# Kernel optimization log

Measured on AMD Instinct MI355X. Metric: run time of the kernel, lower is better.

The kernel has to match this reference:

```python
import jax, jax.numpy as jnp
import numpy as np
from jax import lax

B, L, CIN, COUT, K, H, W = 16, 4, 256, 256, 3, 32, 32
STRIDE, PAD, DIL = 1, 1, 1


def setup_inputs() -> dict:
    key = jax.random.key(0)
    ks = jax.random.split(key, 7)
    x = jax.random.normal(ks[0], (B, L, CIN, H, W), dtype=jnp.float32)
    # base conv weight, stored squeezed from torch shape (1,1,COUT,CIN,K,K)
    weight = jax.random.normal(ks[1], (COUT, CIN, K, K), dtype=jnp.float32) * 0.02
    bias = jax.random.normal(ks[2], (COUT,), dtype=jnp.float32) * 0.02
    # temporalconv: Conv3d(CIN, CIN, (3,1,1)) -> 1D conv over temporal axis
    tconv_w = jax.random.normal(ks[3], (CIN, CIN, 3), dtype=jnp.float32) * 0.02
    tconv_b = jax.random.normal(ks[4], (CIN,), dtype=jnp.float32) * 0.02
    # fc: Conv3d(CIN, 1, (3,1,1))
    fc_w = jax.random.normal(ks[5], (1, CIN, 3), dtype=jnp.float32) * 0.02
    fc_b = jax.random.normal(ks[6], (1,), dtype=jnp.float32) * 0.02
    return {"x": x, "weight": weight, "bias": bias, "tconv_w": tconv_w,
            "tconv_b": tconv_b, "fc_w": fc_w, "fc_b": fc_b}


def _conv1d(inp, w):
    # inp: (b, c_in, t), w: (c_out, c_in, 3), VALID padding -> (b, c_out, t-2)
    return lax.conv_general_dilated(inp, w, window_strides=(1,), padding='VALID',
                                    dimension_numbers=('NCH', 'OIH', 'NCH'))


def reference(x, weight, bias, tconv_w, tconv_b, fc_w, fc_b):
    b, l, c, h, w = x.shape
    # AdaptiveAvgPool3d((None,1,1)) after permute -> spatial global mean: (b, c, l)
    pooled = x.mean(axis=(3, 4)).transpose(0, 2, 1)
    # duplicate first frame twice along temporal axis: (b, c, l+2)
    allxet = jnp.concatenate([pooled[:, :, :1], pooled[:, :, :1], pooled], axis=2)
    calib = _conv1d(allxet, tconv_w) + tconv_b[None, :, None]      # (b, c, l)
    gate = _conv1d(allxet, fc_w) + fc_b[None, :, None]             # (b, 1, l)
    # per-(sample,frame) channel scale on input channels of base weight
    scale = (calib + 1.0).transpose(0, 2, 1)                       # (b, l, c)
    fw = weight[None, None] * scale[:, :, None, :, None, None]     # (b, l, COUT, CIN, K, K)
    fb = bias[None, None, :] * (gate[:, 0, :] + 1.0)[:, :, None]   # (b, l, COUT)
    n = b * l
    xN = x.reshape(n, c, h, w)
    fwN = fw.reshape(n, COUT, c, K, K)
    pad2 = [(PAD, PAD), (PAD, PAD)]

    def conv_one(xi, wi):  # per-sample conv: groups=b*l trick -> vmapped conv
        return lax.conv_general_dilated(xi[None], wi, (STRIDE, STRIDE), pad2,
                                        rhs_dilation=(DIL, DIL),
                                        dimension_numbers=('NCHW', 'OIHW', 'NCHW'))[0]

    out = jax.vmap(conv_one)(xN, fwN)                              # (n, COUT, H', W')
    out = out + fb.reshape(n, COUT)[:, :, None, None]
    return out
```

## Files before the change

### kernel.cpp

```cpp
#include <hip/hip_runtime.h>
#include <hip/hip_bf16.h>

#define CIN 256
#define COUT 256
#define HH 32
#define WW 32
#define LL 4
#define NN 64

typedef unsigned short u16;
typedef __attribute__((ext_vector_type(8))) short short8;
typedef __attribute__((ext_vector_type(4))) float f32x4;

typedef const __attribute__((address_space(1))) void gvoid_t;
typedef __attribute__((address_space(3))) void svoid_t;

static __device__ __forceinline__ u16 f2bf(float f) {
    __hip_bfloat16 h = __float2bfloat16(f);
    return *reinterpret_cast<u16*>(&h);
}
static __device__ __forceinline__ float bf2f(u16 b) {
    unsigned int u = ((unsigned int)b) << 16;
    return __uint_as_float(u);
}

__global__ __launch_bounds__(256) void prep_kernel(const float* __restrict__ x,
                                                   const float* __restrict__ weight,
                                                   const float* __restrict__ tconv_w,
                                                   float* __restrict__ pooled,
                                                   u16* __restrict__ xb,
                                                   u16* __restrict__ wb,
                                                   float* __restrict__ twt) {
    int bx = blockIdx.x;
    int tid = threadIdx.x;
    __shared__ float red[4][8];

    if (bx < 2048) {
        int n = bx >> 5, ko = bx & 31;
        int lane = tid & 63, wave = tid >> 6;
        const float* xn = x + ((size_t)n * CIN + ko * 8) * (HH * WW);

        float psum[8];
        #pragma unroll
        for (int ci = 0; ci < 8; ci++) psum[ci] = 0.f;

        size_t base = ((size_t)n * 32 + ko) * (34 * 34);
        #pragma unroll
        for (int k = 0; k < 4; k++) {
            int pos = k * 256 + tid;
            int h = pos >> 5, w = pos & 31;
            short8 u;
            #pragma unroll
            for (int ci = 0; ci < 8; ci++) {
                float f = xn[ci * (HH * WW) + pos];
                psum[ci] += f;
                u[ci] = (short)f2bf(f);
            }
            *(short8*)(xb + (base + (size_t)(h + 1) * 34 + (w + 1)) * 8) = u;
        }
        if (tid < 132) {
            int cell = tid;
            int hp, wp;
            if (cell < 34)       { hp = 0;              wp = cell; }
            else if (cell < 68)  { hp = 33;             wp = cell - 34; }
            else if (cell < 100) { hp = cell - 68 + 1;  wp = 0; }
            else                 { hp = cell - 100 + 1; wp = 33; }
            short8 z = (short8){0, 0, 0, 0, 0, 0, 0, 0};
            *(short8*)(xb + (base + (size_t)hp * 34 + wp) * 8) = z;
        }
        #pragma unroll
        for (int ci = 0; ci < 8; ci++) {
            float s = psum[ci];
            #pragma unroll
            for (int off = 32; off > 0; off >>= 1) s += __shfl_down(s, off, 64);
            if (lane == 0) red[wave][ci] = s;
        }
        __syncthreads();
        if (tid < 8) {
            pooled[n * CIN + ko * 8 + tid] =
                (red[0][tid] + red[1][tid] + red[2][tid] + red[3][tid]) * (1.0f / (HH * WW));
        }
    } else if (bx < 2304) {
        int co = bx - 2048;
        int ci = tid;
        #pragma unroll
        for (int k = 0; k < 9; k++) {
            u16 v = f2bf(weight[((size_t)co * CIN + ci) * 9 + k]);
            size_t unit = ((size_t)k * 32 + (ci >> 3)) * COUT + co;
            wb[unit * 8 + (ci & 7)] = v;
        }
    } else {
        int co = bx - 2304;
        #pragma unroll
        for (int r = 0; r < 3; r++) {
            int idx = r * 256 + tid;
            int ci = idx / 3, k = idx - ci * 3;
            twt[((size_t)k * 256 + ci) * 256 + co] = tconv_w[(size_t)co * 768 + idx];
        }
    }
}

__global__ __launch_bounds__(256) void calib2_kernel(const float* __restrict__ pooled,
                                                     const float* __restrict__ twt,
                                                     const float* __restrict__ tconv_b,
                                                     const float* __restrict__ fc_w,
                                                     const float* __restrict__ fc_b,
                                                     float* __restrict__ scale,
                                                     float* __restrict__ gmul) {
    int n = blockIdx.x >> 2, coq = blockIdx.x & 3;
    int b = n / LL, t = n % LL;
    int i0 = max(t - 2, 0), i1 = max(t - 1, 0), i2 = t;
    __shared__ float p[3][CIN];
    __shared__ float red[4][64];
    int tid = threadIdx.x;
    p[0][tid] = pooled[(b * LL + i0) * CIN + tid];
    p[1][tid] = pooled[(b * LL + i1) * CIN + tid];
    p[2][tid] = pooled[(b * LL + i2) * CIN + tid];
    __syncthreads();
    int co = coq * 64 + (tid & 63);
    int c0 = (tid >> 6) * 64;
    float acc = 0.f;
    #pragma unroll 4
    for (int i = 0; i < 64; i++) {
        int ci = c0 + i;
        acc += p[0][ci] * twt[(size_t)(0 * 256 + ci) * 256 + co]
             + p[1][ci] * twt[(size_t)(1 * 256 + ci) * 256 + co]
             + p[2][ci] * twt[(size_t)(2 * 256 + ci) * 256 + co];
    }
    red[tid >> 6][tid & 63] = acc;
    __syncthreads();
    if (tid < 64) {
        float a = red[0][tid] + red[1][tid] + red[2][tid] + red[3][tid];
        scale[n * CIN + coq * 64 + tid] = a + tconv_b[coq * 64 + tid] + 1.0f;
    }
    if (coq == 0) {
        const float* fw = fc_w + tid * 3;
        float g = p[0][tid] * fw[0] + p[1][tid] * fw[1] + p[2][tid] * fw[2];
        #pragma unroll
        for (int off = 32; off > 0; off >>= 1) g += __shfl_down(g, off, 64);
        __shared__ float gw[4];
        if ((tid & 63) == 0) gw[tid >> 6] = g;
        __syncthreads();
        if (tid == 0) gmul[n] = gw[0] + gw[1] + gw[2] + gw[3] + fc_b[0] + 1.0f;
    }
}

#define AUNITS 2376
#define BUNITS 2560

__global__ __launch_bounds__(256, 2) void conv_mfma_kernel(
    const u16* __restrict__ xb, const u16* __restrict__ wb,
    const float* __restrict__ scale,
    const float* __restrict__ bias, const float* __restrict__ gmul,
    float* __restrict__ out) {
    int blk = (blockIdx.x & 7) * 64 + (blockIdx.x >> 3);
    int n = blk >> 3, cog = (blk >> 1) & 3, pg = blk & 1;
    int r0 = pg * 16;
    int tid = threadIdx.x;
    int lane = tid & 63, wave = tid >> 6;
    int l15 = lane & 15, l4 = lane >> 4;
    int w4 = wave * 4;

    __shared__ short8 Alds[AUNITS];
    __shared__ short8 Blds[BUNITS];
    __shared__ float scale_lds[CIN];

    scale_lds[tid] = scale[n * CIN + tid];

    f32x4 acc[4][4][2];
    #pragma unroll
    for (int m = 0; m < 4; m++)
        #pragma unroll
        for (int r = 0; r < 4; r++)
            #pragma unroll
            for (int ch = 0; ch < 2; ch++) acc[m][r][ch] = (f32x4){0.f, 0.f, 0.f, 0.f};

    int a_src = wave * 256 + cog * 64 + lane;
    int b_off[10];
    #pragma unroll
    for (int r = 0; r < 10; r++) {
        int u = r * 256 + tid;
        int ue = u < 2455 ? u : 2455;
        int k8 = ue / 614;
        int rem = ue - k8 * 614;
        if (rem > 611) rem = 611;
        b_off[r] = k8 * 1156 + rem;
    }
    int b_base0 = n * 36992 + r0 * 34;

    for (int kc = 0; kc < 8; kc++) {
        __syncthreads();
        #pragma unroll
        for (int r = 0; r < 10; r++) {
            size_t gu = (size_t)(b_base0 + kc * 4624 + b_off[r]);
            __builtin_amdgcn_global_load_lds((gvoid_t*)(xb + gu * 8),
                (svoid_t*)&Blds[r * 256 + wave * 64], 16, 0, 0);
        }
        f32x4 s_lo = *(const f32x4*)&scale_lds[kc * 32 + wave * 8];
        f32x4 s_hi = *(const f32x4*)&scale_lds[kc * 32 + wave * 8 + 4];
        short8 wv[9];
        #pragma unroll
        for (int r = 0; r < 9; r++) {
            size_t gu = (size_t)(r * 8192 + kc * 1024 + a_src);
            wv[r] = *(const short8*)(wb + gu * 8);
        }
        #pragma unroll
        for (int r = 0; r < 9; r++) {
            short8 o;
            #pragma unroll
            for (int e = 0; e < 8; e++) {
                float s = (e < 4) ? s_lo[e] : s_hi[e - 4];
                o[e] = (short)f2bf(bf2f((u16)wv[r][e]) * s);
            }
            Alds[(r * 4 + wave) * 66 + lane] = o;
        }
        __syncthreads();

        #pragma unroll
        for (int dw = 0; dw < 3; dw++) {
            short8 bfr[6][2];
            #pragma unroll
            for (int j = 0; j < 6; j++)
                #pragma unroll
                for (int ch = 0; ch < 2; ch++) {
                    int u = l4 * 614 + (w4 + j) * 34 + ch * 16 + l15 + dw;
                    bfr[j][ch] = Blds[u];
                }
            #pragma unroll
            for (int dh = 0; dh < 3; dh++) {
                int tap = dh * 3 + dw;
                #pragma unroll
                for (int m = 0; m < 4; m++) {
                    int ua = (tap * 4 + l4) * 66 + m * 16 + l15;
                    short8 af = Alds[ua];
                    #pragma unroll
                    for (int r = 0; r < 4; r++)
                        #pragma unroll
                        for (int ch = 0; ch < 2; ch++)
                            acc[m][r][ch] = __builtin_amdgcn_mfma_f32_16x16x32_bf16(
                                af, bfr[r + dh][ch], acc[m][r][ch], 0, 0, 0);
                }
            }
        }
    }

    float gm = gmul[n];
    #pragma unroll
    for (int m = 0; m < 4; m++) {
        #pragma unroll
        for (int r = 0; r < 4; r++) {
            int orow = r0 + w4 + r;
            #pragma unroll
            for (int ch = 0; ch < 2; ch++) {
                #pragma unroll
                for (int j = 0; j < 4; j++) {
                    int co = cog * 64 + m * 16 + l4 * 4 + j;
                    out[(((size_t)n * COUT + co) * HH + orow) * WW + ch * 16 + l15] =
                        acc[m][r][ch][j] + bias[co] * gm;
                }
            }
        }
    }
}

__global__ __launch_bounds__(256) void pool_kernel(const float* __restrict__ x,
                                                   float* __restrict__ pooled) {
    int blk = blockIdx.x;
    const float* src = x + (size_t)blk * (HH * WW);
    int tid = threadIdx.x;
    float4 v = ((const float4*)src)[tid];
    float s = v.x + v.y + v.z + v.w;
    #pragma unroll
    for (int off = 32; off > 0; off >>= 1) s += __shfl_down(s, off, 64);
    __shared__ float ws[4];
    if ((tid & 63) == 0) ws[tid >> 6] = s;
    __syncthreads();
    if (tid == 0) pooled[blk] = (ws[0] + ws[1] + ws[2] + ws[3]) * (1.0f / (HH * WW));
}

__global__ __launch_bounds__(256) void calib_kernel(const float* __restrict__ pooled,
                                                    const float* __restrict__ tconv_w,
                                                    const float* __restrict__ tconv_b,
                                                    const float* __restrict__ fc_w,
                                                    const float* __restrict__ fc_b,
                                                    float* __restrict__ scale,
                                                    float* __restrict__ gmul) {
    int n = blockIdx.x;
    int b = n / LL, t = n % LL;
    int i0 = max(t - 2, 0), i1 = max(t - 1, 0), i2 = t;
    __shared__ float p[3][CIN];
    int tid = threadIdx.x;
    p[0][tid] = pooled[(b * LL + i0) * CIN + tid];
    p[1][tid] = pooled[(b * LL + i1) * CIN + tid];
    p[2][tid] = pooled[(b * LL + i2) * CIN + tid];
    __syncthreads();
    float acc = 0.f;
    for (int ci = 0; ci < CIN; ci++) {
        const float* w = tconv_w + ((size_t)tid * CIN + ci) * 3;
        acc += p[0][ci] * w[0] + p[1][ci] * w[1] + p[2][ci] * w[2];
    }
    scale[n * CIN + tid] = acc + tconv_b[tid] + 1.0f;
    const float* fw = fc_w + tid * 3;
    float g = p[0][tid] * fw[0] + p[1][tid] * fw[1] + p[2][tid] * fw[2];
    #pragma unroll
    for (int off = 32; off > 0; off >>= 1) g += __shfl_down(g, off, 64);
    __shared__ float gw[4];
    if ((tid & 63) == 0) gw[tid >> 6] = g;
    __syncthreads();
    if (tid == 0) gmul[n] = gw[0] + gw[1] + gw[2] + gw[3] + fc_b[0] + 1.0f;
}

__global__ __launch_bounds__(256) void conv_kernel(const float* __restrict__ x,
                                                   const float* __restrict__ weight,
                                                   const float* __restrict__ bias,
                                                   const float* __restrict__ scale,
                                                   const float* __restrict__ gmul,
                                                   float* __restrict__ out) {
    int blk = blockIdx.x;
    int n   = blk >> 5;
    int cog = (blk >> 3) & 3;
    int rg  = blk & 7;
    int co_base  = cog * 64;
    int row_base = rg * 4;
    int tid = threadIdx.x;
    int c   = tid & 31;
    int sub = tid >> 5;

    __shared__ float xin[6][34];
    __shared__ float wsh[9][65];

    float acc[8][4];
    #pragma unroll
    for (int j = 0; j < 8; j++)
        #pragma unroll
        for (int g = 0; g < 4; g++) acc[j][g] = 0.f;

    const float* xn = x + (size_t)n * CIN * HH * WW;

    for (int ci = 0; ci < CIN; ci++) {
        if (tid < 204) {
            float s = scale[n * CIN + ci];
            int lr = tid / 34, lc = tid % 34;
            int gr = row_base - 1 + lr, gc = lc - 1;
            float v = 0.f;
            if (gr >= 0 && gr < HH && gc >= 0 && gc < WW)
                v = xn[(size_t)ci * (HH * WW) + gr * WW + gc] * s;
            xin[lr][lc] = v;
        }
        for (int idx = tid; idx < 576; idx += 256) {
            int co = idx / 9, k = idx % 9;
            wsh[k][co] = weight[(size_t)(co_base + co) * (CIN * 9) + ci * 9 + k];
        }
        __syncthreads();
        float xr[6][3];
        #pragma unroll
        for (int r = 0; r < 6; r++)
            #pragma unroll
            for (int kw = 0; kw < 3; kw++) xr[r][kw] = xin[r][c + kw];
        #pragma unroll
        for (int j = 0; j < 8; j++) {
            float wv[9];
            #pragma unroll
            for (int k = 0; k < 9; k++) wv[k] = wsh[k][sub * 8 + j];
            #pragma unroll
            for (int g = 0; g < 4; g++)
                #pragma unroll
                for (int kh = 0; kh < 3; kh++)
                    #pragma unroll
                    for (int kw = 0; kw < 3; kw++)
                        acc[j][g] += xr[g + kh][kw] * wv[kh * 3 + kw];
        }
        __syncthreads();
    }
    float gm = gmul[n];
    #pragma unroll
    for (int j = 0; j < 8; j++) {
        int co = co_base + sub * 8 + j;
        float fb = bias[co] * gm;
        #pragma unroll
        for (int g = 0; g < 4; g++)
            out[(((size_t)n * COUT + co) * HH + (row_base + g)) * WW + c] = acc[j][g] + fb;
    }
}

extern "C" void kernel_launch(void* const* d_in, const int* in_sizes, int n_in,
                              void* d_out, int out_size, void* d_ws, size_t ws_size,
                              hipStream_t stream) {
    const float* x       = (const float*)d_in[0];
    const float* weight  = (const float*)d_in[1];
    const float* bias    = (const float*)d_in[2];
    const float* tconv_w = (const float*)d_in[3];
    const float* tconv_b = (const float*)d_in[4];
    const float* fc_w    = (const float*)d_in[5];
    const float* fc_b    = (const float*)d_in[6];
    float* out = (float*)d_out;

    char* wsb = (char*)d_ws;
    float* pooled = (float*)wsb;
    float* scale  = pooled + NN * CIN;
    float* gmul   = scale + NN * CIN;
    const size_t XB_OFF = 131328;
    const size_t XB_BYTES = (size_t)NN * 32 * 34 * 34 * 8 * 2;
    const size_t WB_OFF = XB_OFF + XB_BYTES;
    const size_t WB_BYTES = (size_t)9 * 32 * COUT * 8 * 2;
    const size_t TWT_OFF = WB_OFF + WB_BYTES;
    const size_t TWT_BYTES = (size_t)3 * 256 * 256 * 4;
    u16* xb = (u16*)(wsb + XB_OFF);
    u16* wb = (u16*)(wsb + WB_OFF);
    float* twt = (float*)(wsb + TWT_OFF);

    if (ws_size >= TWT_OFF + TWT_BYTES) {
        prep_kernel<<<2560, 256, 0, stream>>>(x, weight, tconv_w, pooled, xb, wb, twt);
        calib2_kernel<<<NN * 4, 256, 0, stream>>>(pooled, twt, tconv_b, fc_w, fc_b, scale, gmul);
        conv_mfma_kernel<<<NN * 4 * 2, 256, 0, stream>>>(xb, wb, scale, bias, gmul, out);
    } else {
        pool_kernel<<<NN * CIN, 256, 0, stream>>>(x, pooled);
        calib_kernel<<<NN, 256, 0, stream>>>(pooled, tconv_w, tconv_b, fc_w, fc_b, scale, gmul);
        conv_kernel<<<NN * 32, 256, 0, stream>>>(x, weight, bias, scale, gmul, out);
    }
}
```

Baseline: 93.07 us.

## Fold channel scale into input activations instead of per-sample weights

The per-(sample,frame) input-channel scale is now applied to the activations while they are converted to padded bf16, in a new kernel that runs after the calibration kernel. The first prep kernel only pools. The conv kernel no longer rescales weights into LDS each K-chunk and reads the shared bf16 weights straight from global memory into MFMA operands. This removes per-block weight scaling and the A tile in LDS, which frees LDS and conversion ALU work. The cost is a second full read of x in an extra launch, and A fragments now come from global or L2 memory inside the MFMA loop.

```diff
diff --git a/kernel.cpp b/kernel.cpp
--- a/kernel.cpp
+++ b/kernel.cpp
@@ -19,18 +19,13 @@
     __hip_bfloat16 h = __float2bfloat16(f);
     return *reinterpret_cast<u16*>(&h);
 }
-static __device__ __forceinline__ float bf2f(u16 b) {
-    unsigned int u = ((unsigned int)b) << 16;
-    return __uint_as_float(u);
-}
-
-__global__ __launch_bounds__(256) void prep_kernel(const float* __restrict__ x,
-                                                   const float* __restrict__ weight,
-                                                   const float* __restrict__ tconv_w,
-                                                   float* __restrict__ pooled,
-                                                   u16* __restrict__ xb,
-                                                   u16* __restrict__ wb,
-                                                   float* __restrict__ twt) {
+
+__global__ __launch_bounds__(256) void pool_prep_kernel(const float* __restrict__ x,
+                                                        const float* __restrict__ weight,
+                                                        const float* __restrict__ tconv_w,
+                                                        float* __restrict__ pooled,
+                                                        u16* __restrict__ wb,
+                                                        float* __restrict__ twt) {
     int bx = blockIdx.x;
     int tid = threadIdx.x;
     __shared__ float red[4][8];
@@ -39,34 +34,11 @@
         int n = bx >> 5, ko = bx & 31;
         int lane = tid & 63, wave = tid >> 6;
         const float* xn = x + ((size_t)n * CIN + ko * 8) * (HH * WW);
-
         float psum[8];
         #pragma unroll
-        for (int ci = 0; ci < 8; ci++) psum[ci] = 0.f;
-
-        size_t base = ((size_t)n * 32 + ko) * (34 * 34);
-        #pragma unroll
-        for (int k = 0; k < 4; k++) {
-            int pos = k * 256 + tid;
-            int h = pos >> 5, w = pos & 31;
-            short8 u;
-            #pragma unroll
-            for (int ci = 0; ci < 8; ci++) {
-                float f = xn[ci * (HH * WW) + pos];
-                psum[ci] += f;
-                u[ci] = (short)f2bf(f);
-            }
-            *(short8*)(xb + (base + (size_t)(h + 1) * 34 + (w + 1)) * 8) = u;
-        }
-        if (tid < 132) {
-            int cell = tid;
-            int hp, wp;
-            if (cell < 34)       { hp = 0;              wp = cell; }
-            else if (cell < 68)  { hp = 33;             wp = cell - 34; }
-            else if (cell < 100) { hp = cell - 68 + 1;  wp = 0; }
-            else                 { hp = cell - 100 + 1; wp = 33; }
-            short8 z = (short8){0, 0, 0, 0, 0, 0, 0, 0};
-            *(short8*)(xb + (base + (size_t)hp * 34 + wp) * 8) = z;
+        for (int ci = 0; ci < 8; ci++) {
+            float4 v = ((const float4*)(xn + ci * (HH * WW)))[tid];
+            psum[ci] = v.x + v.y + v.z + v.w;
         }
         #pragma unroll
         for (int ci = 0; ci < 8; ci++) {
@@ -145,12 +117,47 @@
     }
 }
 
-#define AUNITS 2376
+__global__ __launch_bounds__(256) void xs_prep_kernel(const float* __restrict__ x,
+                                                      const float* __restrict__ scale,
+                                                      u16* __restrict__ xb) {
+    int bx = blockIdx.x;
+    int n = bx >> 5, ko = bx & 31;
+    int tid = threadIdx.x;
+    const float* xn = x + ((size_t)n * CIN + ko * 8) * (HH * WW);
+
+    float sc[8];
+    #pragma unroll
+    for (int ci = 0; ci < 8; ci++) sc[ci] = scale[n * CIN + ko * 8 + ci];
+
+    size_t base = ((size_t)n * 32 + ko) * (34 * 34);
+    #pragma unroll
+    for (int k = 0; k < 4; k++) {
+        int pos = k * 256 + tid;
+        int h = pos >> 5, w = pos & 31;
+        short8 u;
+        #pragma unroll
+        for (int ci = 0; ci < 8; ci++) {
+            float f = xn[ci * (HH * WW) + pos] * sc[ci];
+            u[ci] = (short)f2bf(f);
+        }
+        *(short8*)(xb + (base + (size_t)(h + 1) * 34 + (w + 1)) * 8) = u;
+    }
+    if (tid < 132) {
+        int cell = tid;
+        int hp, wp;
+        if (cell < 34)       { hp = 0;              wp = cell; }
+        else if (cell < 68)  { hp = 33;             wp = cell - 34; }
+        else if (cell < 100) { hp = cell - 68 + 1;  wp = 0; }
+        else                 { hp = cell - 100 + 1; wp = 33; }
+        short8 z = (short8){0, 0, 0, 0, 0, 0, 0, 0};
+        *(short8*)(xb + (base + (size_t)hp * 34 + wp) * 8) = z;
+    }
+}
+
 #define BUNITS 2560
 
 __global__ __launch_bounds__(256, 2) void conv_mfma_kernel(
     const u16* __restrict__ xb, const u16* __restrict__ wb,
-    const float* __restrict__ scale,
     const float* __restrict__ bias, const float* __restrict__ gmul,
     float* __restrict__ out) {
     int blk = (blockIdx.x & 7) * 64 + (blockIdx.x >> 3);
@@ -161,11 +168,7 @@
     int l15 = lane & 15, l4 = lane >> 4;
     int w4 = wave * 4;
 
-    __shared__ short8 Alds[AUNITS];
     __shared__ short8 Blds[BUNITS];
-    __shared__ float scale_lds[CIN];
-
-    scale_lds[tid] = scale[n * CIN + tid];
 
     f32x4 acc[4][4][2];
     #pragma unroll
@@ -175,7 +178,6 @@
             #pragma unroll
             for (int ch = 0; ch < 2; ch++) acc[m][r][ch] = (f32x4){0.f, 0.f, 0.f, 0.f};
 
-    int a_src = wave * 256 + cog * 64 + lane;
     int b_off[10];
     #pragma unroll
     for (int r = 0; r < 10; r++) {
@@ -188,6 +190,8 @@
     }
     int b_base0 = n * 36992 + r0 * 34;
 
+    const u16* wbl = wb + (size_t)(cog * 64 + l15) * 8 + (size_t)l4 * 256 * 8;
+
     for (int kc = 0; kc < 8; kc++) {
         __syncthreads();
         #pragma unroll
@@ -195,24 +199,6 @@
             size_t gu = (size_t)(b_base0 + kc * 4624 + b_off[r]);
             __builtin_amdgcn_global_load_lds((gvoid_t*)(xb + gu * 8),
                 (svoid_t*)&Blds[r * 256 + wave * 64], 16, 0, 0);
-        }
-        f32x4 s_lo = *(const f32x4*)&scale_lds[kc * 32 + wave * 8];
-        f32x4 s_hi = *(const f32x4*)&scale_lds[kc * 32 + wave * 8 + 4];
-        short8 wv[9];
-        #pragma unroll
-        for (int r = 0; r < 9; r++) {
-            size_t gu = (size_t)(r * 8192 + kc * 1024 + a_src);
-            wv[r] = *(const short8*)(wb + gu * 8);
-        }
-        #pragma unroll
-        for (int r = 0; r < 9; r++) {
-            short8 o;
-            #pragma unroll
-            for (int e = 0; e < 8; e++) {
-                float s = (e < 4) ? s_lo[e] : s_hi[e - 4];
-                o[e] = (short)f2bf(bf2f((u16)wv[r][e]) * s);
-            }
-            Alds[(r * 4 + wave) * 66 + lane] = o;
         }
         __syncthreads();
 
@@ -228,18 +214,20 @@
                 }
             #pragma unroll
             for (int dh = 0; dh < 3; dh++) {
-                int tap = dh * 3 + dw;
+                const int tap = dh * 3 + dw;
+                short8 af[4];
                 #pragma unroll
-                for (int m = 0; m < 4; m++) {
-                    int ua = (tap * 4 + l4) * 66 + m * 16 + l15;
-                    short8 af = Alds[ua];
+                for (int m = 0; m < 4; m++)
+                    af[m] = *(const short8*)(wbl +
+                        ((size_t)(tap * 32 + kc * 4) * 256 + m * 16) * 8);
+                #pragma unroll
+                for (int m = 0; m < 4; m++)
                     #pragma unroll
                     for (int r = 0; r < 4; r++)
                         #pragma unroll
                         for (int ch = 0; ch < 2; ch++)
                             acc[m][r][ch] = __builtin_amdgcn_mfma_f32_16x16x32_bf16(
-                                af, bfr[r + dh][ch], acc[m][r][ch], 0, 0, 0);
-                }
+                                af[m], bfr[r + dh][ch], acc[m][r][ch], 0, 0, 0);
             }
         }
     }
@@ -410,9 +398,10 @@
     float* twt = (float*)(wsb + TWT_OFF);
 
     if (ws_size >= TWT_OFF + TWT_BYTES) {
-        prep_kernel<<<2560, 256, 0, stream>>>(x, weight, tconv_w, pooled, xb, wb, twt);
+        pool_prep_kernel<<<2560, 256, 0, stream>>>(x, weight, tconv_w, pooled, wb, twt);
         calib2_kernel<<<NN * 4, 256, 0, stream>>>(pooled, twt, tconv_b, fc_w, fc_b, scale, gmul);
-        conv_mfma_kernel<<<NN * 4 * 2, 256, 0, stream>>>(xb, wb, scale, bias, gmul, out);
+        xs_prep_kernel<<<NN * 32, 256, 0, stream>>>(x, scale, xb);
+        conv_mfma_kernel<<<NN * 4 * 2, 256, 0, stream>>>(xb, wb, bias, gmul, out);
     } else {
         pool_kernel<<<NN * CIN, 256, 0, stream>>>(x, pooled);
         calib_kernel<<<NN, 256, 0, stream>>>(pooled, tconv_w, tconv_b, fc_w, fc_b, scale, gmul);
```

Result: slower. 110.5 us (+18.7%).

## Restructure conv MFMA kernel with double-buffered per-tap pipeline and full-COUT tiles

Applied to the files above, without the earlier changes.

The implicit-GEMM conv kernel now uses 512-thread blocks, each computing all 256 output channels for 8 output rows, instead of 64 channels by 16 rows. The K loop runs per filter tap within 64-channel chunks. Weight (A) tiles are double-buffered per tap and input (B) tiles per chunk, so staging the next tile overlaps MFMA work on the current one. This re-reads the shared input halo less often across channel groups and hides load latency. The costs are fewer blocks (256), one block per CU, and two barriers per tap.

```diff
diff --git a/kernel.cpp b/kernel.cpp
--- a/kernel.cpp
+++ b/kernel.cpp
@@ -145,116 +145,144 @@
     }
 }
 
-#define AUNITS 2376
-#define BUNITS 2560
-
-__global__ __launch_bounds__(256, 2) void conv_mfma_kernel(
+#define AU2 2064
+#define BU2 2752
+
+__global__ __launch_bounds__(512, 1) void conv_mfma_kernel(
     const u16* __restrict__ xb, const u16* __restrict__ wb,
     const float* __restrict__ scale,
     const float* __restrict__ bias, const float* __restrict__ gmul,
     float* __restrict__ out) {
-    int blk = (blockIdx.x & 7) * 64 + (blockIdx.x >> 3);
-    int n = blk >> 3, cog = (blk >> 1) & 3, pg = blk & 1;
-    int r0 = pg * 16;
+    int blk = ((blockIdx.x & 7) << 5) + (blockIdx.x >> 3);
+    int n = blk >> 2, pg = blk & 3;
+    int r0 = pg * 8;
     int tid = threadIdx.x;
     int lane = tid & 63, wave = tid >> 6;
     int l15 = lane & 15, l4 = lane >> 4;
-    int w4 = wave * 4;
-
-    __shared__ short8 Alds[AUNITS];
-    __shared__ short8 Blds[BUNITS];
+    int wm = wave >> 2, wn = wave & 3;
+
+    __shared__ short8 smem[2 * AU2 + 2 * BU2];
     __shared__ float scale_lds[CIN];
-
-    scale_lds[tid] = scale[n * CIN + tid];
-
-    f32x4 acc[4][4][2];
-    #pragma unroll
-    for (int m = 0; m < 4; m++)
-        #pragma unroll
-        for (int r = 0; r < 4; r++)
+    short8* A0 = smem;
+    short8* A1 = smem + AU2;
+    short8* B0 = smem + 2 * AU2;
+    short8* B1 = smem + 2 * AU2 + BU2;
+
+    if (tid < 256) scale_lds[tid] = scale[n * CIN + tid];
+
+    f32x4 acc[8][2][2];
+    #pragma unroll
+    for (int m = 0; m < 8; m++)
+        #pragma unroll
+        for (int r = 0; r < 2; r++)
             #pragma unroll
             for (int ch = 0; ch < 2; ch++) acc[m][r][ch] = (f32x4){0.f, 0.f, 0.f, 0.f};
 
-    int a_src = wave * 256 + cog * 64 + lane;
-    int b_off[10];
-    #pragma unroll
-    for (int r = 0; r < 10; r++) {
-        int u = r * 256 + tid;
-        int ue = u < 2455 ? u : 2455;
-        int k8 = ue / 614;
-        int rem = ue - k8 * 614;
-        if (rem > 611) rem = 611;
-        b_off[r] = k8 * 1156 + rem;
-    }
-    int b_base0 = n * 36992 + r0 * 34;
-
-    for (int kc = 0; kc < 8; kc++) {
-        __syncthreads();
-        #pragma unroll
-        for (int r = 0; r < 10; r++) {
-            size_t gu = (size_t)(b_base0 + kc * 4624 + b_off[r]);
-            __builtin_amdgcn_global_load_lds((gvoid_t*)(xb + gu * 8),
-                (svoid_t*)&Blds[r * 256 + wave * 64], 16, 0, 0);
-        }
-        f32x4 s_lo = *(const f32x4*)&scale_lds[kc * 32 + wave * 8];
-        f32x4 s_hi = *(const f32x4*)&scale_lds[kc * 32 + wave * 8 + 4];
-        short8 wv[9];
-        #pragma unroll
-        for (int r = 0; r < 9; r++) {
-            size_t gu = (size_t)(r * 8192 + kc * 1024 + a_src);
-            wv[r] = *(const short8*)(wb + gu * 8);
-        }
-        #pragma unroll
-        for (int r = 0; r < 9; r++) {
-            short8 o;
-            #pragma unroll
-            for (int e = 0; e < 8; e++) {
-                float s = (e < 4) ? s_lo[e] : s_hi[e - 4];
-                o[e] = (short)f2bf(bf2f((u16)wv[r][e]) * s);
-            }
-            Alds[(r * 4 + wave) * 66 + lane] = o;
-        }
-        __syncthreads();
-
-        #pragma unroll
-        for (int dw = 0; dw < 3; dw++) {
-            short8 bfr[6][2];
-            #pragma unroll
-            for (int j = 0; j < 6; j++)
-                #pragma unroll
-                for (int ch = 0; ch < 2; ch++) {
-                    int u = l4 * 614 + (w4 + j) * 34 + ch * 16 + l15 + dw;
-                    bfr[j][ch] = Blds[u];
-                }
-            #pragma unroll
-            for (int dh = 0; dh < 3; dh++) {
-                int tap = dh * 3 + dw;
-                #pragma unroll
-                for (int m = 0; m < 4; m++) {
-                    int ua = (tap * 4 + l4) * 66 + m * 16 + l15;
-                    short8 af = Alds[ua];
-                    #pragma unroll
-                    for (int r = 0; r < 4; r++)
-                        #pragma unroll
-                        for (int ch = 0; ch < 2; ch++)
-                            acc[m][r][ch] = __builtin_amdgcn_mfma_f32_16x16x32_bf16(
-                                af, bfr[r + dh][ch], acc[m][r][ch], 0, 0, 0);
-                }
-            }
-        }
-    }
+    int bsrc[6];
+    #pragma unroll
+    for (int r = 0; r < 6; r++) {
+        int u = (r * 8 + wave) * 64 + lane;
+        int ue = u < 2735 ? u : 2735;
+        int k8 = ue / 342;
+        int rem = ue - k8 * 342;
+        if (rem > 339) rem = 339;
+        bsrc[r] = k8 * 1156 + r0 * 34 + rem;
+    }
+    int b_base = n * 36992;
+
+    #define STAGE_B(dst, kc4_) do {                                                     \
+        _Pragma("unroll")                                                               \
+        for (int r = 0; r < 6; r++) {                                                   \
+            int c = r * 8 + wave;                                                       \
+            if (c < 43) {                                                               \
+                size_t gu = (size_t)(b_base + (kc4_) * 9248 + bsrc[r]);                 \
+                __builtin_amdgcn_global_load_lds((gvoid_t*)(xb + gu * 8),               \
+                    (svoid_t*)&(dst)[c * 64], 16, 0, 0);                                \
+            }                                                                           \
+        }                                                                               \
+    } while (0)
+
+    #define A_WRITE(dst, tap_, kc4_) do {                                               \
+        _Pragma("unroll")                                                               \
+        for (int r = 0; r < 4; r++) {                                                   \
+            int u = r * 512 + tid;                                                      \
+            int ko = u >> 8, co = u & 255;                                              \
+            size_t gu = ((size_t)((tap_) * 32 + (kc4_) * 8 + ko)) * 256 + co;           \
+            short8 wv = *(const short8*)(wb + gu * 8);                                  \
+            f32x4 s0 = *(const f32x4*)&scale_lds[(kc4_) * 64 + ko * 8];                 \
+            f32x4 s1 = *(const f32x4*)&scale_lds[(kc4_) * 64 + ko * 8 + 4];             \
+            short8 o;                                                                   \
+            _Pragma("unroll")                                                           \
+            for (int e = 0; e < 8; e++) {                                               \
+                float s = (e < 4) ? s0[e] : s1[e - 4];                                  \
+                o[e] = (short)f2bf(bf2f((u16)wv[e]) * s);                               \
+            }                                                                           \
+            (dst)[ko * 258 + co] = o;                                                   \
+        }                                                                               \
+    } while (0)
+
+    #define COMPUTE(t_, Ab, Bb) do {                                                    \
+        const int dh = (t_) / 3, dw = (t_) % 3;                                         \
+        _Pragma("unroll")                                                               \
+        for (int ks = 0; ks < 2; ks++) {                                                \
+            short8 bfr[2][2];                                                           \
+            _Pragma("unroll")                                                           \
+            for (int r = 0; r < 2; r++)                                                 \
+                _Pragma("unroll")                                                       \
+                for (int ch = 0; ch < 2; ch++) {                                        \
+                    int u = (ks * 4 + l4) * 342 + (wn * 2 + r + dh) * 34                \
+                          + ch * 16 + l15 + dw;                                         \
+                    bfr[r][ch] = (Bb)[u];                                               \
+                }                                                                       \
+            _Pragma("unroll")                                                           \
+            for (int m = 0; m < 8; m++) {                                               \
+                short8 af = (Ab)[(ks * 4 + l4) * 258 + wm * 128 + m * 16 + l15];        \
+                _Pragma("unroll")                                                       \
+                for (int r = 0; r < 2; r++)                                             \
+                    _Pragma("unroll")                                                   \
+                    for (int ch = 0; ch < 2; ch++)                                      \
+                        acc[m][r][ch] = __builtin_amdgcn_mfma_f32_16x16x32_bf16(        \
+                            af, bfr[r][ch], acc[m][r][ch], 0, 0, 0);                    \
+            }                                                                           \
+        }                                                                               \
+    } while (0)
+
+    __syncthreads();
+    STAGE_B(B0, 0);
+    A_WRITE(A0, 0, 0);
+    __syncthreads();
+
+    for (int kc4 = 0; kc4 < 4; kc4++) {
+        short8* Bcur = (kc4 & 1) ? B1 : B0;
+        short8* Bnx  = (kc4 & 1) ? B0 : B1;
+        #pragma unroll
+        for (int t = 0; t < 9; t++) {
+            int phase = kc4 * 9 + t;
+            short8* Acur = (phase & 1) ? A1 : A0;
+            short8* Anx  = (phase & 1) ? A0 : A1;
+            if (t == 0 && kc4 < 3) STAGE_B(Bnx, kc4 + 1);
+            if (t < 8)            A_WRITE(Anx, t + 1, kc4);
+            else if (kc4 < 3)     A_WRITE(Anx, 0, kc4 + 1);
+            __syncthreads();
+            COMPUTE(t, Acur, Bcur);
+            __syncthreads();
+        }
+    }
+    #undef COMPUTE
+    #undef A_WRITE
+    #undef STAGE_B
 
     float gm = gmul[n];
     #pragma unroll
-    for (int m = 0; m < 4; m++) {
-        #pragma unroll
-        for (int r = 0; r < 4; r++) {
-            int orow = r0 + w4 + r;
+    for (int m = 0; m < 8; m++) {
+        #pragma unroll
+        for (int r = 0; r < 2; r++) {
+            int orow = r0 + wn * 2 + r;
             #pragma unroll
             for (int ch = 0; ch < 2; ch++) {
                 #pragma unroll
                 for (int j = 0; j < 4; j++) {
-                    int co = cog * 64 + m * 16 + l4 * 4 + j;
+                    int co = wm * 128 + m * 16 + l4 * 4 + j;
                     out[(((size_t)n * COUT + co) * HH + orow) * WW + ch * 16 + l15] =
                         acc[m][r][ch][j] + bias[co] * gm;
                 }
@@ -412,7 +440,7 @@
     if (ws_size >= TWT_OFF + TWT_BYTES) {
         prep_kernel<<<2560, 256, 0, stream>>>(x, weight, tconv_w, pooled, xb, wb, twt);
         calib2_kernel<<<NN * 4, 256, 0, stream>>>(pooled, twt, tconv_b, fc_w, fc_b, scale, gmul);
-        conv_mfma_kernel<<<NN * 4 * 2, 256, 0, stream>>>(xb, wb, scale, bias, gmul, out);
+        conv_mfma_kernel<<<NN * 4, 512, 0, stream>>>(xb, wb, scale, bias, gmul, out);
     } else {
         pool_kernel<<<NN * CIN, 256, 0, stream>>>(x, pooled);
         calib_kernel<<<NN, 256, 0, stream>>>(pooled, tconv_w, tconv_b, fc_w, fc_b, scale, gmul);
```

Result: slower. 190.9 us (+105.1%).
